# Optimization experiments

Hardware: AMD Instinct MI355X
Metric: run time of the kernel (lower is better)

## Reference

```python
import jax, jax.numpy as jnp
import numpy as np

S = 1024      # flattened hierarchical sequence length
D = 1024      # n_embd
H = 16        # n_head
HD = D // H   # head dim (64)
NL = 6        # n_layer
DFF = 4 * D
EPS = 1.1920929e-07  # torch rms_norm default eps (float32 machine eps)


def setup_inputs() -> dict:
    key = jax.random.key(0)
    ks = jax.random.split(key, 12)
    s = 0.02
    return {
        "x": jax.random.normal(ks[0], (1, S, D), jnp.float32),
        "Wq": jax.random.normal(ks[1], (NL, D, D), jnp.float32) * s,
        "Wk": jax.random.normal(ks[2], (NL, D, D), jnp.float32) * s,
        "Wv": jax.random.normal(ks[3], (NL, D, D), jnp.float32) * s,
        "Wo": jax.random.normal(ks[4], (NL, D, D), jnp.float32) * s,
        "lamb": jnp.full((NL,), 0.5, jnp.float32),
        "lambdas": jnp.tile(jnp.array([1.0, 0.0], jnp.float32), (NL, 1)),
        "Wfc": jax.random.normal(ks[5], (NL, DFF, D), jnp.float32) * s,
        "Wp": jax.random.normal(ks[6], (NL, D, DFF), jnp.float32) * s,
        "levels": jax.random.randint(ks[7], (S,), 0, 3, jnp.int32),
        "sample_idx": jnp.sort(jax.random.randint(ks[8], (S,), 0, 8, jnp.int32)),
    }


def rms(t):
    return t * jax.lax.rsqrt(jnp.mean(t * t, axis=-1, keepdims=True) + EPS)


def rope(t):
    # t: [B, T, H, hd]; torch-style half-split rotary
    hd = t.shape[-1]
    d = hd // 2
    inv = 1.0 / (10000.0 ** (jnp.arange(0, hd, 2, dtype=jnp.float32) / hd))
    fr = jnp.outer(jnp.arange(t.shape[1], dtype=jnp.float32), inv)  # [T, d]
    cos = jnp.cos(fr)[None, :, None, :]
    sin = jnp.sin(fr)[None, :, None, :]
    x1, x2 = t[..., :d], t[..., d:]
    return jnp.concatenate([x1 * cos + x2 * sin, -x1 * sin + x2 * cos], axis=-1)


def markov_mask(levels, sample_idx):
    # allowed(q,kv) = causal & same-sample & NOT(levels[kv]==0 and a level-0
    # token exists strictly between kv and q). Equivalent to the torch
    # markov_causal_mask, computed via a cumsum instead of torch.any.
    n = levels.shape[0]
    pos = jnp.arange(n)
    causal = pos[:, None] >= pos[None, :]
    same = sample_idx[:, None] == sample_idx[None, :]
    c = jnp.cumsum((levels == 0).astype(jnp.int32))
    cpad = jnp.concatenate([jnp.zeros((1,), jnp.int32), c])  # cpad[i]=#l0 in [0,i)
    # count of level-0 tokens at positions p with kv < p < q
    cnt = cpad[pos[:, None]] - cpad[pos[None, :] + 1]
    markov = (levels[None, :] == 0) & (cnt > 0)
    return causal & same & ~markov


def reference(x, Wq, Wk, Wv, Wo, lamb, lambdas, Wfc, Wp, levels, sample_idx):
    mask = markov_mask(levels, sample_idx)[None, None]  # [1,1,S,S]
    scale = HD ** -0.5
    neg = jnp.float32(-1e30)

    x = rms(x)          # norm of the hierarchical-trajectory embedding
    x0 = x
    v1 = None
    for i in range(NL):
        xl = lambdas[i, 0] * x + lambdas[i, 1] * x0
        xn = rms(xl)
        B, T = xn.shape[0], xn.shape[1]
        q = (xn @ Wq[i].T).reshape(B, T, H, HD)
        k = (xn @ Wk[i].T).reshape(B, T, H, HD)
        v = (xn @ Wv[i].T).reshape(B, T, H, HD)
        if v1 is None:
            v1 = v
        v = (1.0 - lamb[i]) * v + lamb[i] * v1   # value residual
        q, k = rms(q), rms(k)                    # QK RMSNorm
        q, k = rope(q), rope(k)
        scores = jnp.einsum("bqhd,bkhd->bhqk", q, k) * scale
        scores = jnp.where(mask, scores, neg)
        p = jax.nn.softmax(scores, axis=-1)
        y = jnp.einsum("bhqk,bkhd->bqhd", p, v).reshape(B, T, D)
        x = xl + y @ Wo[i].T
        h = rms(x) @ Wfc[i].T
        h = jnp.square(jax.nn.relu(h))           # relu(x)^2 activation
        x = x + h @ Wp[i].T
    return rms(x)
```

## Files before the change

kernel.cpp:

```cpp
#include <hip/hip_runtime.h>

#define SQ 1024
#define DM 1024
#define NH 16
#define HD 64
#define NL 6
#define DFF 4096
#define EPS 1.1920929e-07f

typedef __attribute__((ext_vector_type(8))) short short8;
typedef __attribute__((ext_vector_type(4))) float floatx4;
typedef __attribute__((address_space(1))) const unsigned int GU32;
typedef __attribute__((address_space(3))) unsigned int LU32;

__device__ __forceinline__ unsigned short f2b(float f) {
    union { float f; unsigned int u; } x; x.f = f;
    unsigned int r = x.u + 0x7fffu + ((x.u >> 16) & 1u);
    return (unsigned short)(r >> 16);
}

__device__ __forceinline__ float wsum(float v) {
#pragma unroll
    for (int m = 32; m >= 1; m >>= 1) v += __shfl_xor(v, m, 64);
    return v;
}
__device__ __forceinline__ float bsum(float v) {
    __shared__ float sh[4];
    v = wsum(v);
    __syncthreads();
    if ((threadIdx.x & 63) == 0) sh[threadIdx.x >> 6] = v;
    __syncthreads();
    return sh[0] + sh[1] + sh[2] + sh[3];
}

__global__ void convert_all(const float* __restrict__ s0, const float* __restrict__ s1,
                            const float* __restrict__ s2, const float* __restrict__ s3,
                            const float* __restrict__ s4, const float* __restrict__ s5,
                            unsigned short* __restrict__ d0, unsigned short* __restrict__ d1,
                            unsigned short* __restrict__ d2, unsigned short* __restrict__ d3,
                            unsigned short* __restrict__ d4, unsigned short* __restrict__ d5) {
    const long ns = (long)NL * DM * DM / 4;
    const long nb = (long)NL * DFF * DM / 4;
    const long total = 4 * ns + 2 * nb;
    long i = (long)blockIdx.x * 256 + threadIdx.x;
    long stride = (long)gridDim.x * 256;
    for (; i < total; i += stride) {
        const float* src; unsigned short* dst; long off;
        if (i < 4 * ns) {
            long seg = i / ns; off = i - seg * ns;
            src = (seg == 0) ? s0 : (seg == 1) ? s1 : (seg == 2) ? s2 : s3;
            dst = (seg == 0) ? d0 : (seg == 1) ? d1 : (seg == 2) ? d2 : d3;
        } else {
            long j = i - 4 * ns;
            if (j < nb) { src = s4; dst = d4; off = j; }
            else        { src = s5; dst = d5; off = j - nb; }
        }
        float4 v = ((const float4*)src)[off];
        ushort4 o;
        o.x = f2b(v.x); o.y = f2b(v.y); o.z = f2b(v.z); o.w = f2b(v.w);
        ((ushort4*)dst)[off] = o;
    }
}

__global__ void scan_levels(const int* __restrict__ levels, int* __restrict__ cpad) {
    __shared__ int sh[SQ];
    int t = threadIdx.x;
    sh[t] = (levels[t] == 0) ? 1 : 0;
    __syncthreads();
    for (int off = 1; off < SQ; off <<= 1) {
        int v = (t >= off) ? sh[t - off] : 0;
        __syncthreads();
        sh[t] += v;
        __syncthreads();
    }
    cpad[t + 1] = sh[t];
    if (t == 0) cpad[0] = 0;
}

__global__ void build_mask_bits(const int* __restrict__ levels, const int* __restrict__ sidx,
                                const int* __restrict__ cpad, unsigned long long* __restrict__ mb) {
    int i = blockIdx.x * 256 + threadIdx.x;
    int q = i >> 10, k = i & 1023;
    bool causal = q >= k;
    bool same = sidx[q] == sidx[k];
    int cnt = cpad[q] - cpad[k + 1];
    bool markov = (levels[k] == 0) && (cnt > 0);
    bool pred = causal && same && !markov;
    unsigned long long bal = __ballot(pred);
    if ((threadIdx.x & 63) == 0) mb[(size_t)q * 16 + (k >> 6)] = bal;
}

__global__ void rms_kernel(const float* __restrict__ in, float* o1, float* o2, unsigned short* ob) {
    int row = blockIdx.x, t = threadIdx.x;
    const float* rp = in + (size_t)row * DM;
    float v[4]; float ss = 0.f;
#pragma unroll
    for (int j = 0; j < 4; ++j) { v[j] = rp[t + j * 256]; ss += v[j] * v[j]; }
    ss = bsum(ss);
    float inv = rsqrtf(ss / (float)DM + EPS);
#pragma unroll
    for (int j = 0; j < 4; ++j) {
        float o = v[j] * inv;
        int c = t + j * 256;
        if (o1) o1[(size_t)row * DM + c] = o;
        if (o2) o2[(size_t)row * DM + c] = o;
        if (ob) ob[(size_t)row * DM + c] = f2b(o);
    }
}

__global__ void xl_rms(const float* __restrict__ x, const float* __restrict__ x0,
                       const float* __restrict__ lam2, float* __restrict__ xl,
                       unsigned short* __restrict__ xnb) {
    int row = blockIdx.x, t = threadIdx.x;
    float l0 = lam2[0], l1 = lam2[1];
    const float* xp = x + (size_t)row * DM;
    const float* x0p = x0 + (size_t)row * DM;
    float v[4]; float ss = 0.f;
#pragma unroll
    for (int j = 0; j < 4; ++j) {
        int c = t + j * 256;
        v[j] = l0 * xp[c] + l1 * x0p[c];
        ss += v[j] * v[j];
    }
    ss = bsum(ss);
    float inv = rsqrtf(ss / (float)DM + EPS);
#pragma unroll
    for (int j = 0; j < 4; ++j) {
        int c = t + j * 256;
        xl[(size_t)row * DM + c] = v[j];
        xnb[(size_t)row * DM + c] = f2b(v[j] * inv);
    }
}

__global__ void qkv_post(const float* __restrict__ qf, const float* __restrict__ kf,
                         unsigned short* __restrict__ qb, unsigned short* __restrict__ kb,
                         const float* __restrict__ vf, float* __restrict__ v1,
                         unsigned short* __restrict__ vt, const float* __restrict__ lambp,
                         int first) {
    __shared__ unsigned short tile[64 * 65];
    int b = blockIdx.x;
    int t = threadIdx.x;
    if (b < 8192) {
        int wid = b * 4 + (t >> 6);
        int lane = t & 63;
        int which = wid >> 14;
        int idx = wid & 16383;
        int s = idx >> 4;
        int h = idx & 15;
        const float* src = (which ? kf : qf) + (size_t)s * DM + h * HD;
        float v = src[lane];
        float ss = v * v;
#pragma unroll
        for (int m = 32; m >= 1; m >>= 1) ss += __shfl_xor(ss, m, 64);
        v *= rsqrtf(ss / (float)HD + EPS);
        float partner = __shfl_xor(v, 32, 64);
        int j = lane & 31;
        float invf = expf(-((float)(2 * j) / (float)HD) * 9.210340371976184f);
        float fr = (float)s * invf;
        float c = cosf(fr), sn = sinf(fr);
        float o = v * c + ((lane < 32) ? sn : -sn) * partner;
        unsigned short* dst = (which ? kb : qb);
        dst[(size_t)s * DM + h * HD + lane] = f2b(o);
    } else {
        int bb = b - 8192;
        int ts = bb >> 4, tc = bb & 15;
        float l = lambp[0];
#pragma unroll
        for (int j = 0; j < 16; ++j) {
            int idx = j * 256 + t;
            int s = idx >> 6, c = idx & 63;
            size_t gi = (size_t)(ts * 64 + s) * DM + tc * 64 + c;
            float val = vf[gi];
            float v1v;
            if (first) { v1[gi] = val; v1v = val; } else v1v = v1[gi];
            tile[c * 65 + s] = f2b((1.f - l) * val + l * v1v);
        }
        __syncthreads();
#pragma unroll
        for (int j = 0; j < 16; ++j) {
            int idx = j * 256 + t;
            int c = idx >> 6, s = idx & 63;
            vt[(size_t)(tc * 64 + c) * SQ + ts * 64 + s] = tile[c * 65 + s];
        }
    }
}

__global__ void reduce_add(float* __restrict__ x, const float* __restrict__ p) {
    int i = blockIdx.x * 256 + threadIdx.x;
    const long n = (long)SQ * DM / 4;
    float4 a = ((const float4*)x)[i];
    float4 p0 = ((const float4*)p)[i];
    float4 p1 = ((const float4*)p)[i + n];
    float4 p2 = ((const float4*)p)[i + 2 * n];
    float4 p3 = ((const float4*)p)[i + 3 * n];
    a.x += p0.x + p1.x + p2.x + p3.x;
    a.y += p0.y + p1.y + p2.y + p3.y;
    a.z += p0.z + p1.z + p2.z + p3.z;
    a.w += p0.w + p1.w + p2.w + p3.w;
    ((float4*)x)[i] = a;
}

__global__ __launch_bounds__(64)
void flash_attn(const unsigned short* __restrict__ qb, const unsigned short* __restrict__ kb,
                const unsigned short* __restrict__ vt, const unsigned long long* __restrict__ mb,
                unsigned short* __restrict__ yb) {
    __shared__ unsigned short Ps[16 * 64];
    int lane = threadIdx.x;
    int qt = blockIdx.x & 63, h = blockIdx.x >> 6;
    int q0 = qt * 16;
    int r = lane & 15, q4 = lane >> 4;
    const unsigned short* qp = qb + (size_t)(q0 + r) * DM + h * HD + q4 * 8;
    short8 aq0 = *(const short8*)qp;
    short8 aq1 = *(const short8*)(qp + 32);
    floatx4 o[4] = {};
    float m[4] = {-1e30f, -1e30f, -1e30f, -1e30f};
    float l[4] = {0.f, 0.f, 0.f, 0.f};
    int nk = (qt >> 2) + 1;
    for (int kt = 0; kt < nk; ++kt) {
        int k0 = kt * 64;
        unsigned long long mw[4];
#pragma unroll
        for (int j = 0; j < 4; ++j) mw[j] = mb[(size_t)(q0 + q4 * 4 + j) * 16 + kt];
        unsigned long long any = mw[0] | mw[1] | mw[2] | mw[3];
        if (__ballot(any != 0ull) == 0ull) continue;
        short8 bk[4][2], bv[4][2];
#pragma unroll
        for (int ni = 0; ni < 4; ++ni) {
            const unsigned short* kp = kb + (size_t)(k0 + ni * 16 + r) * DM + h * HD + q4 * 8;
            bk[ni][0] = *(const short8*)kp;
            bk[ni][1] = *(const short8*)(kp + 32);
            const unsigned short* vp = vt + (size_t)(h * HD + ni * 16 + r) * SQ + k0 + q4 * 8;
            bv[ni][0] = *(const short8*)vp;
            bv[ni][1] = *(const short8*)(vp + 32);
        }
        float sm[4][4];
#pragma unroll
        for (int ni = 0; ni < 4; ++ni) {
            floatx4 z = {};
            z = __builtin_amdgcn_mfma_f32_16x16x32_bf16(aq0, bk[ni][0], z, 0, 0, 0);
            z = __builtin_amdgcn_mfma_f32_16x16x32_bf16(aq1, bk[ni][1], z, 0, 0, 0);
#pragma unroll
            for (int j = 0; j < 4; ++j) {
                float sv = z[j] * 0.125f;
                bool bit = (mw[j] >> (ni * 16 + r)) & 1ull;
                sm[ni][j] = bit ? sv : -__builtin_inff();
            }
        }
        float alpha[4];
#pragma unroll
        for (int j = 0; j < 4; ++j) {
            float v = fmaxf(fmaxf(sm[0][j], sm[1][j]), fmaxf(sm[2][j], sm[3][j]));
#pragma unroll
            for (int d = 1; d < 16; d <<= 1) v = fmaxf(v, __shfl_xor(v, d, 64));
            float mn = fmaxf(m[j], v);
            alpha[j] = __expf(m[j] - mn);
            m[j] = mn;
        }
        float p[4][4];
        float rs[4] = {0.f, 0.f, 0.f, 0.f};
#pragma unroll
        for (int ni = 0; ni < 4; ++ni)
#pragma unroll
            for (int j = 0; j < 4; ++j) {
                p[ni][j] = __expf(sm[ni][j] - m[j]);
                rs[j] += p[ni][j];
            }
#pragma unroll
        for (int j = 0; j < 4; ++j) {
            float v = rs[j];
#pragma unroll
            for (int d = 1; d < 16; d <<= 1) v += __shfl_xor(v, d, 64);
            l[j] = l[j] * alpha[j] + v;
        }
#pragma unroll
        for (int ni = 0; ni < 4; ++ni)
#pragma unroll
            for (int j = 0; j < 4; ++j) {
                o[ni][j] *= alpha[j];
                Ps[(q4 * 4 + j) * 64 + ni * 16 + r] = f2b(p[ni][j]);
            }
        short8 ap0 = *(const short8*)(Ps + r * 64 + q4 * 8);
        short8 ap1 = *(const short8*)(Ps + r * 64 + 32 + q4 * 8);
#pragma unroll
        for (int ni = 0; ni < 4; ++ni) {
            o[ni] = __builtin_amdgcn_mfma_f32_16x16x32_bf16(ap0, bv[ni][0], o[ni], 0, 0, 0);
            o[ni] = __builtin_amdgcn_mfma_f32_16x16x32_bf16(ap1, bv[ni][1], o[ni], 0, 0, 0);
        }
    }
#pragma unroll
    for (int j = 0; j < 4; ++j) l[j] = 1.f / l[j];
#pragma unroll
    for (int ni = 0; ni < 4; ++ni)
#pragma unroll
        for (int j = 0; j < 4; ++j)
            yb[(size_t)(q0 + q4 * 4 + j) * DM + h * HD + ni * 16 + r] = f2b(o[ni][j] * l[j]);
}

template<int BM, int BN>
__global__ __launch_bounds__(256, 2)
void gemm_t(const unsigned short* __restrict__ A, int lda, long long sA,
            const unsigned short* __restrict__ B, int ldb, long long sB,
            float* Cf, unsigned short* Cb, int ldc, long long sC,
            const float* __restrict__ addsrc, int ldadd,
            int K, float scale, int act) {
    constexpr int BK = 32;
    constexpr int MI = BM / 32, NI = BN / 32;
    constexpr int CA = BM / 16, CB = BN / 16;
    constexpr int CAW = CA / 4, CBW = CB / 4;
    __shared__ unsigned short As[BM * BK];
    __shared__ unsigned short Bs[BN * BK];

    int t = threadIdx.x;
    int wave = t >> 6, lane = t & 63;
    int m0 = blockIdx.y * BM, n0 = blockIdx.x * BN;
    int z = blockIdx.z;
    const unsigned short* Ab = A + (size_t)z * sA;
    const unsigned short* Bb = B + (size_t)z * sB;

    int r = lane & 15, q4 = lane >> 4;
    int sr = lane >> 2, sseg = lane & 3;
    int wmo = (wave >> 1) * (BM / 2);
    int wno = (wave & 1) * (BN / 2);

    floatx4 acc[MI][NI] = {};

    for (int k0 = 0; k0 < K; k0 += BK) {
#pragma unroll
        for (int j = 0; j < CAW; ++j) {
            int c = wave * CAW + j;
            const unsigned short* g = Ab + (size_t)(m0 + c * 16 + sr) * lda + k0 + sseg * 8;
            __builtin_amdgcn_global_load_lds((GU32*)g, (LU32*)(As + c * 512), 16, 0, 0);
        }
#pragma unroll
        for (int j = 0; j < CBW; ++j) {
            int c = wave * CBW + j;
            const unsigned short* g = Bb + (size_t)(n0 + c * 16 + sr) * ldb + k0 + sseg * 8;
            __builtin_amdgcn_global_load_lds((GU32*)g, (LU32*)(Bs + c * 512), 16, 0, 0);
        }
        __syncthreads();

        short8 af[MI], bfr[NI];
#pragma unroll
        for (int mi = 0; mi < MI; ++mi)
            af[mi] = *(const short8*)(As + (wmo + mi * 16 + r) * BK + q4 * 8);
#pragma unroll
        for (int ni = 0; ni < NI; ++ni)
            bfr[ni] = *(const short8*)(Bs + (wno + ni * 16 + r) * BK + q4 * 8);
#pragma unroll
        for (int mi = 0; mi < MI; ++mi)
#pragma unroll
            for (int ni = 0; ni < NI; ++ni)
                acc[mi][ni] = __builtin_amdgcn_mfma_f32_16x16x32_bf16(af[mi], bfr[ni], acc[mi][ni], 0, 0, 0);
        __syncthreads();
    }

    size_t cz = (size_t)z * sC;
#pragma unroll
    for (int mi = 0; mi < MI; ++mi) {
#pragma unroll
        for (int ni = 0; ni < NI; ++ni) {
            int col = n0 + wno + ni * 16 + r;
#pragma unroll
            for (int j = 0; j < 4; ++j) {
                int row = m0 + wmo + mi * 16 + q4 * 4 + j;
                float v = acc[mi][ni][j] * scale;
                if (addsrc) v += addsrc[(size_t)row * ldadd + col];
                if (act == 1) { v = fmaxf(v, 0.f); v = v * v; }
                if (Cf) Cf[cz + (size_t)row * ldc + col] = v;
                if (Cb) Cb[cz + (size_t)row * ldc + col] = f2b(v);
            }
        }
    }
}

extern "C" void kernel_launch(void* const* d_in, const int* in_sizes, int n_in,
                              void* d_out, int out_size, void* d_ws, size_t ws_size,
                              hipStream_t stream) {
    const float* x_in    = (const float*)d_in[0];
    const float* Wq      = (const float*)d_in[1];
    const float* Wk      = (const float*)d_in[2];
    const float* Wv      = (const float*)d_in[3];
    const float* Wo      = (const float*)d_in[4];
    const float* lamb    = (const float*)d_in[5];
    const float* lambdas = (const float*)d_in[6];
    const float* Wfc     = (const float*)d_in[7];
    const float* Wp      = (const float*)d_in[8];
    const int*   levels  = (const int*)d_in[9];
    const int*   sidx    = (const int*)d_in[10];
    float* out = (float*)d_out;

    char* ws = (char*)d_ws;
    size_t off = 0;
    auto alloc = [&](size_t b) { void* p = ws + off; off = (off + b + 255) & ~(size_t)255; return p; };

    unsigned short* wq_b  = (unsigned short*)alloc((size_t)NL * DM * DM * 2);
    unsigned short* wk_b  = (unsigned short*)alloc((size_t)NL * DM * DM * 2);
    unsigned short* wv_b  = (unsigned short*)alloc((size_t)NL * DM * DM * 2);
    unsigned short* wo_b  = (unsigned short*)alloc((size_t)NL * DM * DM * 2);
    unsigned short* wfc_b = (unsigned short*)alloc((size_t)NL * DFF * DM * 2);
    unsigned short* wp_b  = (unsigned short*)alloc((size_t)NL * DM * DFF * 2);
    int* cpad             = (int*)alloc((SQ + 1) * 4);
    unsigned long long* mb = (unsigned long long*)alloc((size_t)SQ * 16 * 8);
    float* x    = (float*)alloc((size_t)SQ * DM * 4);
    float* x0   = (float*)alloc((size_t)SQ * DM * 4);
    float* xl   = (float*)alloc((size_t)SQ * DM * 4);
    float* qf   = (float*)alloc((size_t)SQ * DM * 4);
    float* kf   = (float*)alloc((size_t)SQ * DM * 4);
    float* vf   = (float*)alloc((size_t)SQ * DM * 4);
    float* v1   = (float*)alloc((size_t)SQ * DM * 4);
    float* pp   = (float*)alloc((size_t)4 * SQ * DM * 4);
    unsigned short* xn_b = (unsigned short*)alloc((size_t)SQ * DM * 2);
    unsigned short* qb   = (unsigned short*)alloc((size_t)SQ * DM * 2);
    unsigned short* kb   = (unsigned short*)alloc((size_t)SQ * DM * 2);
    unsigned short* vt   = (unsigned short*)alloc((size_t)SQ * DM * 2);
    unsigned short* y_b  = (unsigned short*)alloc((size_t)SQ * DM * 2);
    unsigned short* xh_b = (unsigned short*)alloc((size_t)SQ * DM * 2);
    unsigned short* h_b  = (unsigned short*)alloc((size_t)SQ * DFF * 2);

    if (off > ws_size) return;

    const long long WSTRIDE = (long long)NL * DM * DM;
    const long long XSTRIDE = (long long)SQ * DM;

    convert_all<<<2048, 256, 0, stream>>>(Wq, Wk, Wv, Wo, Wfc, Wp,
                                          wq_b, wk_b, wv_b, wo_b, wfc_b, wp_b);

    scan_levels<<<1, 1024, 0, stream>>>(levels, cpad);
    build_mask_bits<<<4096, 256, 0, stream>>>(levels, sidx, cpad, mb);

    rms_kernel<<<SQ, 256, 0, stream>>>(x_in, x, x0, nullptr);

    for (int i = 0; i < NL; ++i) {
        xl_rms<<<SQ, 256, 0, stream>>>(x, x0, lambdas + 2 * i, xl, xn_b);

        gemm_t<128, 128><<<dim3(8, 8, 3), 256, 0, stream>>>(
            xn_b, DM, 0, wq_b + (size_t)i * DM * DM, DM, WSTRIDE,
            qf, nullptr, DM, XSTRIDE, nullptr, 0, DM, 1.f, 0);

        qkv_post<<<8448, 256, 0, stream>>>(qf, kf, qb, kb, vf, v1, vt, lamb + i, (i == 0) ? 1 : 0);

        flash_attn<<<1024, 64, 0, stream>>>(qb, kb, vt, mb, y_b);

        gemm_t<64, 64><<<dim3(16, 16, 1), 256, 0, stream>>>(
            y_b, DM, 0, wo_b + (size_t)i * DM * DM, DM, 0,
            x, nullptr, DM, 0, xl, DM, DM, 1.f, 0);

        rms_kernel<<<SQ, 256, 0, stream>>>(x, nullptr, nullptr, xh_b);
        gemm_t<128, 128><<<dim3(32, 8, 1), 256, 0, stream>>>(
            xh_b, DM, 0, wfc_b + (size_t)i * DFF * DM, DM, 0,
            nullptr, h_b, DFF, 0, nullptr, 0, DM, 1.f, 1);
        gemm_t<128, 128><<<dim3(8, 8, 4), 256, 0, stream>>>(
            h_b, DFF, 1024, wp_b + (size_t)i * DM * DFF, DFF, 1024,
            pp, nullptr, DM, (long long)SQ * DM, nullptr, 0, 1024, 1.f, 0);
        reduce_add<<<SQ * DM / 4 / 256, 256, 0, stream>>>(x, pp);
    }

    rms_kernel<<<SQ, 256, 0, stream>>>(x, out, nullptr, nullptr);
}
```

Measured before the change: 1.211 ms.

## Fuse QK norm and RoPE into QKV GEMM, split-K Wo, fuse reductions with RMS

```diff
diff --git a/kernel.cpp b/kernel.cpp
--- a/kernel.cpp
+++ b/kernel.cpp
@@ -39,27 +39,31 @@
                             unsigned short* __restrict__ d0, unsigned short* __restrict__ d1,
                             unsigned short* __restrict__ d2, unsigned short* __restrict__ d3,
                             unsigned short* __restrict__ d4, unsigned short* __restrict__ d5) {
-    const long ns = (long)NL * DM * DM / 4;
-    const long nb = (long)NL * DFF * DM / 4;
-    const long total = 4 * ns + 2 * nb;
-    long i = (long)blockIdx.x * 256 + threadIdx.x;
-    long stride = (long)gridDim.x * 256;
-    for (; i < total; i += stride) {
-        const float* src; unsigned short* dst; long off;
-        if (i < 4 * ns) {
-            long seg = i / ns; off = i - seg * ns;
-            src = (seg == 0) ? s0 : (seg == 1) ? s1 : (seg == 2) ? s2 : s3;
-            dst = (seg == 0) ? d0 : (seg == 1) ? d1 : (seg == 2) ? d2 : d3;
-        } else {
-            long j = i - 4 * ns;
-            if (j < nb) { src = s4; dst = d4; off = j; }
-            else        { src = s5; dst = d5; off = j - nb; }
-        }
-        float4 v = ((const float4*)src)[off];
+    int bid = blockIdx.x;
+    const float* src; unsigned short* dst; long base;
+    if (bid < 3072)        { src = s0; dst = d0; base = (long)bid * 512; }
+    else if (bid < 6144)   { src = s1; dst = d1; base = (long)(bid - 3072) * 512; }
+    else if (bid < 9216)   { src = s2; dst = d2; base = (long)(bid - 6144) * 512; }
+    else if (bid < 12288)  { src = s3; dst = d3; base = (long)(bid - 9216) * 512; }
+    else if (bid < 24576)  { src = s4; dst = d4; base = (long)(bid - 12288) * 512; }
+    else                   { src = s5; dst = d5; base = (long)(bid - 24576) * 512; }
+    long i0 = base + threadIdx.x;
+#pragma unroll
+    for (int u = 0; u < 2; ++u) {
+        long i = i0 + u * 256;
+        float4 v = ((const float4*)src)[i];
         ushort4 o;
         o.x = f2b(v.x); o.y = f2b(v.y); o.z = f2b(v.z); o.w = f2b(v.w);
-        ((ushort4*)dst)[off] = o;
-    }
+        ((ushort4*)dst)[i] = o;
+    }
+}
+
+__global__ void build_rope(float2* __restrict__ tab) {
+    int i = blockIdx.x * 256 + threadIdx.x;
+    int s = i >> 5, d = i & 31;
+    float invf = expf(-((float)(2 * d) / (float)HD) * 9.210340371976184f);
+    float fr = (float)s * invf;
+    tab[i] = make_float2(cosf(fr), sinf(fr));
 }
 
 __global__ void scan_levels(const int* __restrict__ levels, int* __restrict__ cpad) {
@@ -90,114 +94,141 @@
     if ((threadIdx.x & 63) == 0) mb[(size_t)q * 16 + (k >> 6)] = bal;
 }
 
-__global__ void rms_kernel(const float* __restrict__ in, float* o1, float* o2, unsigned short* ob) {
+__global__ void rms0(const float* __restrict__ xin, const float* __restrict__ lam2,
+                     float* __restrict__ x0, float* __restrict__ xl,
+                     unsigned short* __restrict__ xnb) {
     int row = blockIdx.x, t = threadIdx.x;
-    const float* rp = in + (size_t)row * DM;
+    float l0 = lam2[0], l1 = lam2[1];
+    const float* rp = xin + (size_t)row * DM;
     float v[4]; float ss = 0.f;
 #pragma unroll
     for (int j = 0; j < 4; ++j) { v[j] = rp[t + j * 256]; ss += v[j] * v[j]; }
     ss = bsum(ss);
     float inv = rsqrtf(ss / (float)DM + EPS);
+    float coef = l0 + l1;
+    float w[4]; float ss2 = 0.f;
 #pragma unroll
     for (int j = 0; j < 4; ++j) {
-        float o = v[j] * inv;
-        int c = t + j * 256;
-        if (o1) o1[(size_t)row * DM + c] = o;
-        if (o2) o2[(size_t)row * DM + c] = o;
-        if (ob) ob[(size_t)row * DM + c] = f2b(o);
-    }
-}
-
-__global__ void xl_rms(const float* __restrict__ x, const float* __restrict__ x0,
-                       const float* __restrict__ lam2, float* __restrict__ xl,
-                       unsigned short* __restrict__ xnb) {
-    int row = blockIdx.x, t = threadIdx.x;
-    float l0 = lam2[0], l1 = lam2[1];
-    const float* xp = x + (size_t)row * DM;
-    const float* x0p = x0 + (size_t)row * DM;
-    float v[4]; float ss = 0.f;
+        float r = v[j] * inv;
+        x0[(size_t)row * DM + t + j * 256] = r;
+        w[j] = coef * r;
+        ss2 += w[j] * w[j];
+    }
+    ss2 = bsum(ss2);
+    float inv2 = rsqrtf(ss2 / (float)DM + EPS);
 #pragma unroll
     for (int j = 0; j < 4; ++j) {
-        int c = t + j * 256;
-        v[j] = l0 * xp[c] + l1 * x0p[c];
-        ss += v[j] * v[j];
-    }
-    ss = bsum(ss);
-    float inv = rsqrtf(ss / (float)DM + EPS);
-#pragma unroll
-    for (int j = 0; j < 4; ++j) {
-        int c = t + j * 256;
-        xl[(size_t)row * DM + c] = v[j];
-        xnb[(size_t)row * DM + c] = f2b(v[j] * inv);
-    }
-}
-
-__global__ void qkv_post(const float* __restrict__ qf, const float* __restrict__ kf,
-                         unsigned short* __restrict__ qb, unsigned short* __restrict__ kb,
-                         const float* __restrict__ vf, float* __restrict__ v1,
-                         unsigned short* __restrict__ vt, const float* __restrict__ lambp,
-                         int first) {
+        size_t idx = (size_t)row * DM + t + j * 256;
+        xl[idx] = w[j];
+        xnb[idx] = f2b(w[j] * inv2);
+    }
+}
+
+__global__ __launch_bounds__(256, 2)
+void gemm_qkv(const unsigned short* __restrict__ A,
+              const unsigned short* __restrict__ B0,
+              long long sB,
+              unsigned short* __restrict__ qb, unsigned short* __restrict__ kb,
+              float* __restrict__ vf,
+              const float2* __restrict__ rope) {
+    constexpr int BM = 64, BN = 128, BK = 32;
+    __shared__ unsigned short As[BM * BK];
+    __shared__ unsigned short Bs[BN * BK];
+    int t = threadIdx.x, wave = t >> 6, lane = t & 63;
+    int m0 = blockIdx.y * BM, n0 = blockIdx.x * BN;
+    int z = blockIdx.z;
+    const unsigned short* Bb = B0 + (size_t)z * sB;
+    int r = lane & 15, q4 = lane >> 4;
+    int sr = lane >> 2, sseg = lane & 3;
+    int wmo = (wave >> 1) * 32, wno = (wave & 1) * 64;
+
+    floatx4 acc[2][4] = {};
+    for (int k0 = 0; k0 < DM; k0 += BK) {
+        {
+            int c = wave;
+            const unsigned short* g = A + (size_t)(m0 + c * 16 + sr) * DM + k0 + sseg * 8;
+            __builtin_amdgcn_global_load_lds((GU32*)g, (LU32*)(As + c * 512), 16, 0, 0);
+        }
+#pragma unroll
+        for (int j = 0; j < 2; ++j) {
+            int c = wave * 2 + j;
+            const unsigned short* g = Bb + (size_t)(n0 + c * 16 + sr) * DM + k0 + sseg * 8;
+            __builtin_amdgcn_global_load_lds((GU32*)g, (LU32*)(Bs + c * 512), 16, 0, 0);
+        }
+        __syncthreads();
+        short8 af[2], bfr[4];
+#pragma unroll
+        for (int mi = 0; mi < 2; ++mi)
+            af[mi] = *(const short8*)(As + (wmo + mi * 16 + r) * BK + q4 * 8);
+#pragma unroll
+        for (int ni = 0; ni < 4; ++ni)
+            bfr[ni] = *(const short8*)(Bs + (wno + ni * 16 + r) * BK + q4 * 8);
+#pragma unroll
+        for (int mi = 0; mi < 2; ++mi)
+#pragma unroll
+            for (int ni = 0; ni < 4; ++ni)
+                acc[mi][ni] = __builtin_amdgcn_mfma_f32_16x16x32_bf16(af[mi], bfr[ni], acc[mi][ni], 0, 0, 0);
+        __syncthreads();
+    }
+
+    if (z == 2) {
+#pragma unroll
+        for (int mi = 0; mi < 2; ++mi)
+#pragma unroll
+            for (int ni = 0; ni < 4; ++ni)
+#pragma unroll
+                for (int j = 0; j < 4; ++j)
+                    vf[(size_t)(m0 + wmo + mi * 16 + q4 * 4 + j) * DM + n0 + wno + ni * 16 + r] = acc[mi][ni][j];
+        return;
+    }
+    unsigned short* dst = z ? kb : qb;
+#pragma unroll
+    for (int mi = 0; mi < 2; ++mi) {
+#pragma unroll
+        for (int j = 0; j < 4; ++j) {
+            int row = m0 + wmo + mi * 16 + q4 * 4 + j;
+            float v0 = acc[mi][0][j], v1 = acc[mi][1][j], v2 = acc[mi][2][j], v3 = acc[mi][3][j];
+            float ss = v0 * v0 + v1 * v1 + v2 * v2 + v3 * v3;
+#pragma unroll
+            for (int d = 1; d < 16; d <<= 1) ss += __shfl_xor(ss, d, 64);
+            float inv = rsqrtf(ss * (1.f / 64.f) + EPS);
+            v0 *= inv; v1 *= inv; v2 *= inv; v3 *= inv;
+            float2 t0 = rope[row * 32 + r];
+            float2 t1 = rope[row * 32 + 16 + r];
+            size_t rb = (size_t)row * DM + n0 + wno + r;
+            dst[rb]      = f2b(v0 * t0.x + v2 * t0.y);
+            dst[rb + 16] = f2b(v1 * t1.x + v3 * t1.y);
+            dst[rb + 32] = f2b(v2 * t0.x - v0 * t0.y);
+            dst[rb + 48] = f2b(v3 * t1.x - v1 * t1.y);
+        }
+    }
+}
+
+__global__ void v_post(const float* __restrict__ vf, float* __restrict__ v1,
+                       unsigned short* __restrict__ vt, const float* __restrict__ lambp,
+                       int first) {
     __shared__ unsigned short tile[64 * 65];
     int b = blockIdx.x;
     int t = threadIdx.x;
-    if (b < 8192) {
-        int wid = b * 4 + (t >> 6);
-        int lane = t & 63;
-        int which = wid >> 14;
-        int idx = wid & 16383;
-        int s = idx >> 4;
-        int h = idx & 15;
-        const float* src = (which ? kf : qf) + (size_t)s * DM + h * HD;
-        float v = src[lane];
-        float ss = v * v;
-#pragma unroll
-        for (int m = 32; m >= 1; m >>= 1) ss += __shfl_xor(ss, m, 64);
-        v *= rsqrtf(ss / (float)HD + EPS);
-        float partner = __shfl_xor(v, 32, 64);
-        int j = lane & 31;
-        float invf = expf(-((float)(2 * j) / (float)HD) * 9.210340371976184f);
-        float fr = (float)s * invf;
-        float c = cosf(fr), sn = sinf(fr);
-        float o = v * c + ((lane < 32) ? sn : -sn) * partner;
-        unsigned short* dst = (which ? kb : qb);
-        dst[(size_t)s * DM + h * HD + lane] = f2b(o);
-    } else {
-        int bb = b - 8192;
-        int ts = bb >> 4, tc = bb & 15;
-        float l = lambp[0];
-#pragma unroll
-        for (int j = 0; j < 16; ++j) {
-            int idx = j * 256 + t;
-            int s = idx >> 6, c = idx & 63;
-            size_t gi = (size_t)(ts * 64 + s) * DM + tc * 64 + c;
-            float val = vf[gi];
-            float v1v;
-            if (first) { v1[gi] = val; v1v = val; } else v1v = v1[gi];
-            tile[c * 65 + s] = f2b((1.f - l) * val + l * v1v);
-        }
-        __syncthreads();
-#pragma unroll
-        for (int j = 0; j < 16; ++j) {
-            int idx = j * 256 + t;
-            int c = idx >> 6, s = idx & 63;
-            vt[(size_t)(tc * 64 + c) * SQ + ts * 64 + s] = tile[c * 65 + s];
-        }
-    }
-}
-
-__global__ void reduce_add(float* __restrict__ x, const float* __restrict__ p) {
-    int i = blockIdx.x * 256 + threadIdx.x;
-    const long n = (long)SQ * DM / 4;
-    float4 a = ((const float4*)x)[i];
-    float4 p0 = ((const float4*)p)[i];
-    float4 p1 = ((const float4*)p)[i + n];
-    float4 p2 = ((const float4*)p)[i + 2 * n];
-    float4 p3 = ((const float4*)p)[i + 3 * n];
-    a.x += p0.x + p1.x + p2.x + p3.x;
-    a.y += p0.y + p1.y + p2.y + p3.y;
-    a.z += p0.z + p1.z + p2.z + p3.z;
-    a.w += p0.w + p1.w + p2.w + p3.w;
-    ((float4*)x)[i] = a;
+    int ts = b >> 4, tc = b & 15;
+    float l = lambp[0];
+#pragma unroll
+    for (int j = 0; j < 16; ++j) {
+        int idx = j * 256 + t;
+        int s = idx >> 6, c = idx & 63;
+        size_t gi = (size_t)(ts * 64 + s) * DM + tc * 64 + c;
+        float val = vf[gi];
+        float v1v;
+        if (first) { v1[gi] = val; v1v = val; } else v1v = v1[gi];
+        tile[c * 65 + s] = f2b((1.f - l) * val + l * v1v);
+    }
+    __syncthreads();
+#pragma unroll
+    for (int j = 0; j < 16; ++j) {
+        int idx = j * 256 + t;
+        int c = idx >> 6, s = idx & 63;
+        vt[(size_t)(tc * 64 + c) * SQ + ts * 64 + s] = tile[c * 65 + s];
+    }
 }
 
 __global__ __launch_bounds__(64)
@@ -373,6 +404,53 @@
     }
 }
 
+__global__ void wo_rms(const float* __restrict__ xl, const float* __restrict__ pp,
+                       float* __restrict__ x, unsigned short* __restrict__ xhb) {
+    int row = blockIdx.x, t = threadIdx.x;
+    const long n = (long)SQ * DM;
+    size_t base = (size_t)row * DM;
+    float a[4]; float ss = 0.f;
+#pragma unroll
+    for (int j = 0; j < 4; ++j) {
+        size_t idx = base + t + j * 256;
+        float v = xl[idx] + pp[idx] + pp[idx + n];
+        x[idx] = v;
+        a[j] = v; ss += v * v;
+    }
+    ss = bsum(ss);
+    float inv = rsqrtf(ss / (float)DM + EPS);
+#pragma unroll
+    for (int j = 0; j < 4; ++j)
+        xhb[base + t + j * 256] = f2b(a[j] * inv);
+}
+
+__global__ void proj_reduce_xlrms(const float* __restrict__ x, const float* __restrict__ pp,
+                                  const float* __restrict__ x0, const float* __restrict__ lam2,
+                                  float* __restrict__ xl, unsigned short* __restrict__ xnb,
+                                  float* __restrict__ out, int last) {
+    int row = blockIdx.x, t = threadIdx.x;
+    const long n = (long)SQ * DM;
+    size_t base = (size_t)row * DM;
+    float l0 = 0.f, l1 = 0.f;
+    if (!last) { l0 = lam2[0]; l1 = lam2[1]; }
+    float a[4]; float ss = 0.f;
+#pragma unroll
+    for (int j = 0; j < 4; ++j) {
+        size_t idx = base + t + j * 256;
+        float v = x[idx] + pp[idx] + pp[idx + n] + pp[idx + 2 * n] + pp[idx + 3 * n];
+        if (!last) { v = l0 * v + l1 * x0[idx]; xl[idx] = v; }
+        a[j] = v; ss += v * v;
+    }
+    ss = bsum(ss);
+    float inv = rsqrtf(ss / (float)DM + EPS);
+#pragma unroll
+    for (int j = 0; j < 4; ++j) {
+        size_t idx = base + t + j * 256;
+        if (last) out[idx] = a[j] * inv;
+        else xnb[idx] = f2b(a[j] * inv);
+    }
+}
+
 extern "C" void kernel_launch(void* const* d_in, const int* in_sizes, int n_in,
                               void* d_out, int out_size, void* d_ws, size_t ws_size,
                               hipStream_t stream) {
@@ -401,11 +479,10 @@
     unsigned short* wp_b  = (unsigned short*)alloc((size_t)NL * DM * DFF * 2);
     int* cpad             = (int*)alloc((SQ + 1) * 4);
     unsigned long long* mb = (unsigned long long*)alloc((size_t)SQ * 16 * 8);
+    float2* rope          = (float2*)alloc((size_t)SQ * 32 * 8);
     float* x    = (float*)alloc((size_t)SQ * DM * 4);
     float* x0   = (float*)alloc((size_t)SQ * DM * 4);
     float* xl   = (float*)alloc((size_t)SQ * DM * 4);
-    float* qf   = (float*)alloc((size_t)SQ * DM * 4);
-    float* kf   = (float*)alloc((size_t)SQ * DM * 4);
     float* vf   = (float*)alloc((size_t)SQ * DM * 4);
     float* v1   = (float*)alloc((size_t)SQ * DM * 4);
     float* pp   = (float*)alloc((size_t)4 * SQ * DM * 4);
@@ -422,38 +499,36 @@
     const long long WSTRIDE = (long long)NL * DM * DM;
     const long long XSTRIDE = (long long)SQ * DM;
 
-    convert_all<<<2048, 256, 0, stream>>>(Wq, Wk, Wv, Wo, Wfc, Wp,
-                                          wq_b, wk_b, wv_b, wo_b, wfc_b, wp_b);
+    convert_all<<<36864, 256, 0, stream>>>(Wq, Wk, Wv, Wo, Wfc, Wp,
+                                           wq_b, wk_b, wv_b, wo_b, wfc_b, wp_b);
 
     scan_levels<<<1, 1024, 0, stream>>>(levels, cpad);
     build_mask_bits<<<4096, 256, 0, stream>>>(levels, sidx, cpad, mb);
-
-    rms_kernel<<<SQ, 256, 0, stream>>>(x_in, x, x0, nullptr);
+    build_rope<<<128, 256, 0, stream>>>(rope);
+
+    rms0<<<SQ, 256, 0, stream>>>(x_in, lambdas, x0, xl, xn_b);
 
     for (int i = 0; i < NL; ++i) {
-        xl_rms<<<SQ, 256, 0, stream>>>(x, x0, lambdas + 2 * i, xl, xn_b);
-
-        gemm_t<128, 128><<<dim3(8, 8, 3), 256, 0, stream>>>(
-            xn_b, DM, 0, wq_b + (size_t)i * DM * DM, DM, WSTRIDE,
-            qf, nullptr, DM, XSTRIDE, nullptr, 0, DM, 1.f, 0);
-
-        qkv_post<<<8448, 256, 0, stream>>>(qf, kf, qb, kb, vf, v1, vt, lamb + i, (i == 0) ? 1 : 0);
+        gemm_qkv<<<dim3(8, 16, 3), 256, 0, stream>>>(
+            xn_b, wq_b + (size_t)i * DM * DM, WSTRIDE, qb, kb, vf, rope);
+
+        v_post<<<256, 256, 0, stream>>>(vf, v1, vt, lamb + i, (i == 0) ? 1 : 0);
 
         flash_attn<<<1024, 64, 0, stream>>>(qb, kb, vt, mb, y_b);
 
-        gemm_t<64, 64><<<dim3(16, 16, 1), 256, 0, stream>>>(
-            y_b, DM, 0, wo_b + (size_t)i * DM * DM, DM, 0,
-            x, nullptr, DM, 0, xl, DM, DM, 1.f, 0);
-
-        rms_kernel<<<SQ, 256, 0, stream>>>(x, nullptr, nullptr, xh_b);
-        gemm_t<128, 128><<<dim3(32, 8, 1), 256, 0, stream>>>(
+        gemm_t<64, 64><<<dim3(16, 16, 2), 256, 0, stream>>>(
+            y_b, DM, 512, wo_b + (size_t)i * DM * DM, DM, 512,
+            pp, nullptr, DM, XSTRIDE, nullptr, 0, 512, 1.f, 0);
+        wo_rms<<<SQ, 256, 0, stream>>>(xl, pp, x, xh_b);
+
+        gemm_t<128, 64><<<dim3(64, 8, 1), 256, 0, stream>>>(
             xh_b, DM, 0, wfc_b + (size_t)i * DFF * DM, DM, 0,
             nullptr, h_b, DFF, 0, nullptr, 0, DM, 1.f, 1);
-        gemm_t<128, 128><<<dim3(8, 8, 4), 256, 0, stream>>>(
+        gemm_t<128, 64><<<dim3(16, 8, 4), 256, 0, stream>>>(
             h_b, DFF, 1024, wp_b + (size_t)i * DM * DFF, DFF, 1024,
-            pp, nullptr, DM, (long long)SQ * DM, nullptr, 0, 1024, 1.f, 0);
-        reduce_add<<<SQ * DM / 4 / 256, 256, 0, stream>>>(x, pp);
-    }
-
-    rms_kernel<<<SQ, 256, 0, stream>>>(x, out, nullptr, nullptr);
-}
+            pp, nullptr, DM, XSTRIDE, nullptr, 0, 1024, 1.f, 0);
+        proj_reduce_xlrms<<<SQ, 256, 0, stream>>>(
+            x, pp, x0, (i < NL - 1) ? (lambdas + 2 * (i + 1)) : nullptr,
+            xl, xn_b, out, (i == NL - 1) ? 1 : 0);
+    }
+}
```

Result: faster. 1.027 ms (-15.2%).
